# Performance work log

Hardware: AMD Instinct MI355X
Metric: run time of the kernel (lower is better)

The kernel has to match this reference:

```python
import jax, jax.numpy as jnp
import numpy as np

EPS = 1e-8
NEG_INF = -9e15  # matches torch masked_fill value


def setup_inputs() -> dict:
    key = jax.random.key(0)
    k1, k2 = jax.random.split(key)
    B, D = 4096, 512
    p1 = jax.random.normal(k1, (B, D), dtype=jnp.float32)
    p2 = jax.random.normal(k2, (B, D), dtype=jnp.float32)
    return {"p1": p1, "p2": p2}


def reference(p1, p2):
    # NT-Xent / InfoNCE loss as in SimCLR_MODEL.contrastive_loss (temperature = 1).
    z = jnp.concatenate([p1, p2], axis=0)              # [N, D], N = 2B
    # cosine similarity == GEMM of L2-normalized rows (torch eps clamp = 1e-8)
    zn = z / jnp.maximum(jnp.linalg.norm(z, axis=-1, keepdims=True), EPS)
    sim = zn @ zn.T                                     # [N, N]
    N = sim.shape[0]
    idx = jnp.arange(N)
    sim = sim.at[idx, idx].set(NEG_INF)                 # mask self-similarity
    # positive pair of row i is row (i + N/2) mod N (eye rolled by N/2)
    pos = sim[idx, (idx + N // 2) % N]                  # [N]
    nll = -pos + jax.nn.logsumexp(sim, axis=-1)
    return jnp.mean(nll)
```

## Files before the change

kernel.cpp:

```cpp
#include <hip/hip_runtime.h>
#include <hip/hip_bf16.h>
#include <math.h>

#define N_TOT 8192
#define HALF_N 4096
#define D_DIM 512
#define BM 128
#define BK 64
#define NKIT (D_DIM / BK)
#define NTILES 2080

typedef float f32x4_t __attribute__((ext_vector_type(4)));
typedef long long i64x2 __attribute__((ext_vector_type(2)));

typedef __attribute__((address_space(1))) unsigned int g_u32;
typedef __attribute__((address_space(3))) unsigned int l_u32;

__global__ __launch_bounds__(256) void k_normalize(
    const float* __restrict__ p1, const float* __restrict__ p2,
    unsigned char* __restrict__ zf8, float* __restrict__ rowsum,
    float* __restrict__ out)
{
    const int w = threadIdx.x >> 6;
    const int lane = threadIdx.x & 63;
    const int row = blockIdx.x * 4 + w;

    if (threadIdx.x < 4) rowsum[blockIdx.x * 4 + threadIdx.x] = 0.0f;
    if (blockIdx.x == 0 && threadIdx.x == 0) out[0] = 0.0f;

    const float* src = (row < HALF_N) ? p1 + (size_t)row * D_DIM
                                      : p2 + (size_t)(row - HALF_N) * D_DIM;
    float4 a = *(const float4*)(src + lane * 4);
    float4 b = *(const float4*)(src + 256 + lane * 4);
    float s = a.x*a.x + a.y*a.y + a.z*a.z + a.w*a.w
            + b.x*b.x + b.y*b.y + b.z*b.z + b.w*b.w;
    #pragma unroll
    for (int m = 1; m < 64; m <<= 1) s += __shfl_xor(s, m, 64);
    float inv = 1.0f / fmaxf(sqrtf(s), 1e-8f);

    int pk0 = __builtin_amdgcn_cvt_pk_fp8_f32(a.x * inv, a.y * inv, 0, false);
    pk0     = __builtin_amdgcn_cvt_pk_fp8_f32(a.z * inv, a.w * inv, pk0, true);
    int pk1 = __builtin_amdgcn_cvt_pk_fp8_f32(b.x * inv, b.y * inv, 0, false);
    pk1     = __builtin_amdgcn_cvt_pk_fp8_f32(b.z * inv, b.w * inv, pk1, true);

    unsigned char* dst = zf8 + (size_t)row * D_DIM;
    const int o0 = lane * 4;
    const int o1 = 256 + lane * 4;
    const int d0 = (o0 & ~63) + ((o0 >> 3) & 3) * 16 + ((o0 >> 5) & 1) * 8 + (o0 & 4);
    const int d1 = (o1 & ~63) + ((o1 >> 3) & 3) * 16 + ((o1 >> 5) & 1) * 8 + (o1 & 4);
    *(int*)(dst + d0) = pk0;
    *(int*)(dst + d1) = pk1;
}

__global__ __launch_bounds__(256, 4) void k_gemm(
    const unsigned char* __restrict__ zf8,
    float* __restrict__ rowsum, float* __restrict__ pos)
{
    __shared__ __align__(16) unsigned char As[2][BM * BK];
    __shared__ __align__(16) unsigned char Bs[2][BM * BK];

    const int tid = threadIdx.x;
    const int lane = tid & 63;
    const int w = tid >> 6;
    const int wr = w >> 1, wc = w & 1;
    const int q = lane >> 4, l15 = lane & 15;

    const int t = blockIdx.x;
    int bi = (int)((sqrtf(8.0f * (float)t + 1.0f) - 1.0f) * 0.5f);
    while ((bi + 1) * (bi + 2) / 2 <= t) ++bi;
    while (bi * (bi + 1) / 2 > t) --bi;
    const int bx = bi;
    const int by = t - bi * (bi + 1) / 2;
    const bool isDiag = (bx == by);
    const bool hasPos = (bx - by == 32);
    const int rowBase = by * BM;
    const int colBase = bx * BM;

    const int ci0 = tid;
    const int ci1 = 256 + tid;
    const int r0 = ci0 >> 2, cc0 = ci0 & 3;
    const int r1 = ci1 >> 2, cc1 = ci1 & 3;
    const int gc0 = cc0 ^ ((r0 >> 1) & 3);
    const int gc1 = cc1 ^ ((r1 >> 1) & 3);

    const unsigned char* gA0 = zf8 + (size_t)(rowBase + r0) * D_DIM + gc0 * 16;
    const unsigned char* gA1 = zf8 + (size_t)(rowBase + r1) * D_DIM + gc1 * 16;
    const unsigned char* gB0 = zf8 + (size_t)(colBase + r0) * D_DIM + gc0 * 16;
    const unsigned char* gB1 = zf8 + (size_t)(colBase + r1) * D_DIM + gc1 * 16;

    f32x4_t acc[4][4] = {};

    __builtin_amdgcn_global_load_lds((const g_u32*)gA0, (l_u32*)&As[0][ci0 * 16], 16, 0, 0);
    __builtin_amdgcn_global_load_lds((const g_u32*)gA1, (l_u32*)&As[0][ci1 * 16], 16, 0, 0);
    __builtin_amdgcn_global_load_lds((const g_u32*)gB0, (l_u32*)&Bs[0][ci0 * 16], 16, 0, 0);
    __builtin_amdgcn_global_load_lds((const g_u32*)gB1, (l_u32*)&Bs[0][ci1 * 16], 16, 0, 0);

    #pragma unroll
    for (int it = 0; it < NKIT; it++) {
        const int cur = it & 1;
        __syncthreads();

        if (it + 1 < NKIT) {
            const int kb = (it + 1) * BK;
            const int nxt = 1 - cur;
            __builtin_amdgcn_global_load_lds((const g_u32*)(gA0 + kb), (l_u32*)&As[nxt][ci0 * 16], 16, 0, 0);
            __builtin_amdgcn_global_load_lds((const g_u32*)(gA1 + kb), (l_u32*)&As[nxt][ci1 * 16], 16, 0, 0);
            __builtin_amdgcn_global_load_lds((const g_u32*)(gB0 + kb), (l_u32*)&Bs[nxt][ci0 * 16], 16, 0, 0);
            __builtin_amdgcn_global_load_lds((const g_u32*)(gB1 + kb), (l_u32*)&Bs[nxt][ci1 * 16], 16, 0, 0);
        }

        i64x2 aF[4], bF[4];
        #pragma unroll
        for (int i = 0; i < 4; i++) {
            const int ra = wr * 64 + i * 16 + l15;
            const int rb = wc * 64 + i * 16 + l15;
            aF[i] = *(const i64x2*)&As[cur][ra * BK + (q ^ ((ra >> 1) & 3)) * 16];
            bF[i] = *(const i64x2*)&Bs[cur][rb * BK + (q ^ ((rb >> 1) & 3)) * 16];
        }
        #pragma unroll
        for (int h = 0; h < 2; h++)
            #pragma unroll
            for (int i = 0; i < 4; i++)
                #pragma unroll
                for (int j = 0; j < 4; j++)
                    acc[i][j] = __builtin_amdgcn_mfma_f32_16x16x32_fp8_fp8(
                        aF[i][h], bF[j][h], acc[i][j], 0, 0, 0);
    }

    float colacc[4] = {0.f, 0.f, 0.f, 0.f};
    #pragma unroll
    for (int i = 0; i < 4; i++) {
        #pragma unroll
        for (int r = 0; r < 4; r++) {
            const int row = rowBase + wr * 64 + i * 16 + q * 4 + r;
            float rs = 0.0f;
            #pragma unroll
            for (int j = 0; j < 4; j++) {
                const int col = colBase + wc * 64 + j * 16 + l15;
                const float c = acc[i][j][r];
                float e = __expf(c);
                if (isDiag && col == row) e = 0.0f;
                rs += e;
                colacc[j] += e;
                if (hasPos && col == row + HALF_N) { pos[row] = c; pos[col] = c; }
            }
            rs += __shfl_xor(rs, 1); rs += __shfl_xor(rs, 2);
            rs += __shfl_xor(rs, 4); rs += __shfl_xor(rs, 8);
            if (l15 == 0) atomicAdd(&rowsum[row], rs);
        }
    }
    if (!isDiag) {
        #pragma unroll
        for (int j = 0; j < 4; j++) {
            float cs = colacc[j];
            cs += __shfl_xor(cs, 16);
            cs += __shfl_xor(cs, 32);
            if (q == 0) atomicAdd(&rowsum[colBase + wc * 64 + j * 16 + l15], cs);
        }
    }
}

__global__ __launch_bounds__(256) void k_finalize(
    const float* __restrict__ rowsum, const float* __restrict__ pos,
    float* __restrict__ out)
{
    const int t = threadIdx.x;
    const int i = blockIdx.x * 256 + t;
    float s = logf(rowsum[i]) - pos[i];
    #pragma unroll
    for (int m = 1; m < 64; m <<= 1) s += __shfl_xor(s, m, 64);
    __shared__ float red[4];
    if ((t & 63) == 0) red[t >> 6] = s;
    __syncthreads();
    if (t == 0)
        atomicAdd(out, (red[0] + red[1] + red[2] + red[3]) * (1.0f / (float)N_TOT));
}

extern "C" void kernel_launch(void* const* d_in, const int* in_sizes, int n_in,
                              void* d_out, int out_size, void* d_ws, size_t ws_size,
                              hipStream_t stream) {
    const float* p1 = (const float*)d_in[0];
    const float* p2 = (const float*)d_in[1];

    unsigned char* zf8 = (unsigned char*)d_ws;
    float* rowsum = (float*)((char*)d_ws + (size_t)N_TOT * D_DIM);
    float* pos    = rowsum + N_TOT;
    float* outp   = (float*)d_out;

    k_normalize<<<N_TOT / 4, 256, 0, stream>>>(p1, p2, zf8, rowsum, outp);
    k_gemm<<<NTILES, 256, 0, stream>>>(zf8, rowsum, pos);
    k_finalize<<<N_TOT / 256, 256, 0, stream>>>(rowsum, pos, outp);
}
```

Measured before the change: 106.7 us.

## Triple-buffer LDS tiles with prefetch distance two and partial vmcnt waits

Moves the FP8 GEMM's global-to-LDS pipeline from double to triple buffering. Two K-blocks are issued ahead, and each iteration waits only until the older stage's loads have landed (vmcnt 4) before the barrier, instead of a full __syncthreads drain. The aim is to hide more global-load latency behind MFMA work. In exchange, LDS per block grows from 32KB to 48KB, which may limit blocks per CU under launch_bounds(256,4), and it relies on hand-encoded waitcnt immediates being correct for this ISA.

```diff
diff --git a/kernel.cpp b/kernel.cpp
--- a/kernel.cpp
+++ b/kernel.cpp
@@ -9,6 +9,9 @@
 #define BK 64
 #define NKIT (D_DIM / BK)
 #define NTILES 2080
+
+#define WAIT_VM4 0xF74
+#define WAIT_VM0 0xF70
 
 typedef float f32x4_t __attribute__((ext_vector_type(4)));
 typedef long long i64x2 __attribute__((ext_vector_type(2)));
@@ -56,8 +59,8 @@
     const unsigned char* __restrict__ zf8,
     float* __restrict__ rowsum, float* __restrict__ pos)
 {
-    __shared__ __align__(16) unsigned char As[2][BM * BK];
-    __shared__ __align__(16) unsigned char Bs[2][BM * BK];
+    __shared__ __align__(16) unsigned char As[3][BM * BK];
+    __shared__ __align__(16) unsigned char Bs[3][BM * BK];
 
     const int tid = threadIdx.x;
     const int lane = tid & 63;
@@ -88,26 +91,27 @@
     const unsigned char* gB0 = zf8 + (size_t)(colBase + r0) * D_DIM + gc0 * 16;
     const unsigned char* gB1 = zf8 + (size_t)(colBase + r1) * D_DIM + gc1 * 16;
 
+    auto stage = [&](int buf, int kblk) {
+        const int kb = kblk * BK;
+        __builtin_amdgcn_global_load_lds((const g_u32*)(gA0 + kb), (l_u32*)&As[buf][ci0 * 16], 16, 0, 0);
+        __builtin_amdgcn_global_load_lds((const g_u32*)(gA1 + kb), (l_u32*)&As[buf][ci1 * 16], 16, 0, 0);
+        __builtin_amdgcn_global_load_lds((const g_u32*)(gB0 + kb), (l_u32*)&Bs[buf][ci0 * 16], 16, 0, 0);
+        __builtin_amdgcn_global_load_lds((const g_u32*)(gB1 + kb), (l_u32*)&Bs[buf][ci1 * 16], 16, 0, 0);
+    };
+
     f32x4_t acc[4][4] = {};
 
-    __builtin_amdgcn_global_load_lds((const g_u32*)gA0, (l_u32*)&As[0][ci0 * 16], 16, 0, 0);
-    __builtin_amdgcn_global_load_lds((const g_u32*)gA1, (l_u32*)&As[0][ci1 * 16], 16, 0, 0);
-    __builtin_amdgcn_global_load_lds((const g_u32*)gB0, (l_u32*)&Bs[0][ci0 * 16], 16, 0, 0);
-    __builtin_amdgcn_global_load_lds((const g_u32*)gB1, (l_u32*)&Bs[0][ci1 * 16], 16, 0, 0);
+    stage(0, 0);
+    stage(1, 1);
 
     #pragma unroll
     for (int it = 0; it < NKIT; it++) {
-        const int cur = it & 1;
-        __syncthreads();
+        const int cur = it % 3;
+        if (it + 1 < NKIT) __builtin_amdgcn_s_waitcnt(WAIT_VM4);
+        else               __builtin_amdgcn_s_waitcnt(WAIT_VM0);
+        __builtin_amdgcn_s_barrier();
 
-        if (it + 1 < NKIT) {
-            const int kb = (it + 1) * BK;
-            const int nxt = 1 - cur;
-            __builtin_amdgcn_global_load_lds((const g_u32*)(gA0 + kb), (l_u32*)&As[nxt][ci0 * 16], 16, 0, 0);
-            __builtin_amdgcn_global_load_lds((const g_u32*)(gA1 + kb), (l_u32*)&As[nxt][ci1 * 16], 16, 0, 0);
-            __builtin_amdgcn_global_load_lds((const g_u32*)(gB0 + kb), (l_u32*)&Bs[nxt][ci0 * 16], 16, 0, 0);
-            __builtin_amdgcn_global_load_lds((const g_u32*)(gB1 + kb), (l_u32*)&Bs[nxt][ci1 * 16], 16, 0, 0);
-        }
+        if (it + 2 < NKIT) stage((it + 2) % 3, it + 2);
 
         i64x2 aF[4], bF[4];
         #pragma unroll
```

After: 105.8 us (median of 2 runs). No clear change (-0.8%).

## Use 512-thread blocks with 8 waves splitting the 128x128 GEMM tile

Applied to the files above, without the earlier changes.

The GEMM block grows from 4 to 8 waves: each wave now computes a 32x64 sub-tile instead of 64x64, and each thread issues one global-to-LDS load per matrix per stage instead of two. The aim is more latency hiding and occupancy per CU, since each wave needs fewer accumulator registers. In exchange, every wave re-reads the same B fragments, which raises LDS read traffic per MFMA, and larger blocks pay more per barrier. Column-sum atomics also double, because each of the four row-waves contributes separately.

```diff
diff --git a/kernel.cpp b/kernel.cpp
--- a/kernel.cpp
+++ b/kernel.cpp
@@ -52,7 +52,7 @@
     *(int*)(dst + d1) = pk1;
 }
 
-__global__ __launch_bounds__(256, 4) void k_gemm(
+__global__ __launch_bounds__(512, 6) void k_gemm(
     const unsigned char* __restrict__ zf8,
     float* __restrict__ rowsum, float* __restrict__ pos)
 {
@@ -62,7 +62,8 @@
     const int tid = threadIdx.x;
     const int lane = tid & 63;
     const int w = tid >> 6;
-    const int wr = w >> 1, wc = w & 1;
+    const int wr = w >> 1;
+    const int wc = w & 1;
     const int q = lane >> 4, l15 = lane & 15;
 
     const int t = blockIdx.x;
@@ -76,24 +77,15 @@
     const int rowBase = by * BM;
     const int colBase = bx * BM;
 
-    const int ci0 = tid;
-    const int ci1 = 256 + tid;
-    const int r0 = ci0 >> 2, cc0 = ci0 & 3;
-    const int r1 = ci1 >> 2, cc1 = ci1 & 3;
-    const int gc0 = cc0 ^ ((r0 >> 1) & 3);
-    const int gc1 = cc1 ^ ((r1 >> 1) & 3);
+    const int srow = tid >> 2, scc = tid & 3;
+    const int sgc = scc ^ ((srow >> 1) & 3);
+    const unsigned char* gA = zf8 + (size_t)(rowBase + srow) * D_DIM + sgc * 16;
+    const unsigned char* gB = zf8 + (size_t)(colBase + srow) * D_DIM + sgc * 16;
 
-    const unsigned char* gA0 = zf8 + (size_t)(rowBase + r0) * D_DIM + gc0 * 16;
-    const unsigned char* gA1 = zf8 + (size_t)(rowBase + r1) * D_DIM + gc1 * 16;
-    const unsigned char* gB0 = zf8 + (size_t)(colBase + r0) * D_DIM + gc0 * 16;
-    const unsigned char* gB1 = zf8 + (size_t)(colBase + r1) * D_DIM + gc1 * 16;
+    f32x4_t acc[2][4] = {};
 
-    f32x4_t acc[4][4] = {};
-
-    __builtin_amdgcn_global_load_lds((const g_u32*)gA0, (l_u32*)&As[0][ci0 * 16], 16, 0, 0);
-    __builtin_amdgcn_global_load_lds((const g_u32*)gA1, (l_u32*)&As[0][ci1 * 16], 16, 0, 0);
-    __builtin_amdgcn_global_load_lds((const g_u32*)gB0, (l_u32*)&Bs[0][ci0 * 16], 16, 0, 0);
-    __builtin_amdgcn_global_load_lds((const g_u32*)gB1, (l_u32*)&Bs[0][ci1 * 16], 16, 0, 0);
+    __builtin_amdgcn_global_load_lds((const g_u32*)gA, (l_u32*)&As[0][tid * 16], 16, 0, 0);
+    __builtin_amdgcn_global_load_lds((const g_u32*)gB, (l_u32*)&Bs[0][tid * 16], 16, 0, 0);
 
     #pragma unroll
     for (int it = 0; it < NKIT; it++) {
@@ -103,24 +95,25 @@
         if (it + 1 < NKIT) {
             const int kb = (it + 1) * BK;
             const int nxt = 1 - cur;
-            __builtin_amdgcn_global_load_lds((const g_u32*)(gA0 + kb), (l_u32*)&As[nxt][ci0 * 16], 16, 0, 0);
-            __builtin_amdgcn_global_load_lds((const g_u32*)(gA1 + kb), (l_u32*)&As[nxt][ci1 * 16], 16, 0, 0);
-            __builtin_amdgcn_global_load_lds((const g_u32*)(gB0 + kb), (l_u32*)&Bs[nxt][ci0 * 16], 16, 0, 0);
-            __builtin_amdgcn_global_load_lds((const g_u32*)(gB1 + kb), (l_u32*)&Bs[nxt][ci1 * 16], 16, 0, 0);
+            __builtin_amdgcn_global_load_lds((const g_u32*)(gA + kb), (l_u32*)&As[nxt][tid * 16], 16, 0, 0);
+            __builtin_amdgcn_global_load_lds((const g_u32*)(gB + kb), (l_u32*)&Bs[nxt][tid * 16], 16, 0, 0);
         }
 
-        i64x2 aF[4], bF[4];
+        i64x2 aF[2], bF[4];
         #pragma unroll
-        for (int i = 0; i < 4; i++) {
-            const int ra = wr * 64 + i * 16 + l15;
-            const int rb = wc * 64 + i * 16 + l15;
+        for (int i = 0; i < 2; i++) {
+            const int ra = wr * 32 + i * 16 + l15;
             aF[i] = *(const i64x2*)&As[cur][ra * BK + (q ^ ((ra >> 1) & 3)) * 16];
-            bF[i] = *(const i64x2*)&Bs[cur][rb * BK + (q ^ ((rb >> 1) & 3)) * 16];
+        }
+        #pragma unroll
+        for (int j = 0; j < 4; j++) {
+            const int rb = wc * 64 + j * 16 + l15;
+            bF[j] = *(const i64x2*)&Bs[cur][rb * BK + (q ^ ((rb >> 1) & 3)) * 16];
         }
         #pragma unroll
         for (int h = 0; h < 2; h++)
             #pragma unroll
-            for (int i = 0; i < 4; i++)
+            for (int i = 0; i < 2; i++)
                 #pragma unroll
                 for (int j = 0; j < 4; j++)
                     acc[i][j] = __builtin_amdgcn_mfma_f32_16x16x32_fp8_fp8(
@@ -129,10 +122,10 @@
 
     float colacc[4] = {0.f, 0.f, 0.f, 0.f};
     #pragma unroll
-    for (int i = 0; i < 4; i++) {
+    for (int i = 0; i < 2; i++) {
         #pragma unroll
         for (int r = 0; r < 4; r++) {
-            const int row = rowBase + wr * 64 + i * 16 + q * 4 + r;
+            const int row = rowBase + wr * 32 + i * 16 + q * 4 + r;
             float rs = 0.0f;
             #pragma unroll
             for (int j = 0; j < 4; j++) {
@@ -188,6 +181,6 @@
     float* outp   = (float*)d_out;
 
     k_normalize<<<N_TOT / 4, 256, 0, stream>>>(p1, p2, zf8, rowsum, outp);
-    k_gemm<<<NTILES, 256, 0, stream>>>(zf8, rowsum, pos);
+    k_gemm<<<NTILES, 512, 0, stream>>>(zf8, rowsum, pos);
     k_finalize<<<N_TOT / 256, 256, 0, stream>>>(rowsum, pos, outp);
 }
```

After: 109.9 us. 1.03x slower.
